# Kernel tuning notes

Measured on AMD Instinct MI355X. Metric: run time of the kernel, lower is better.

## Reference

```python
import jax, jax.numpy as jnp
import numpy as np

B, C_IN, T = 4, 256, 8192
LAYERS, STACKS = 24, 4
RES, GATE, SKIP, K = 128, 256, 128, 3
LPS = LAYERS // STACKS  # layers per stack -> dilation = 2**(i % LPS)
SQRT_HALF = 0.7071067811865476


def setup_inputs() -> dict:
    key = jax.random.key(0)
    ks = jax.random.split(key, 14)
    s = 0.08  # small init so the 24-layer stack stays well-scaled
    inp = {
        "x": jax.random.normal(ks[0], (B, C_IN, T), jnp.float32),
        "first_w": jax.random.normal(ks[1], (RES, C_IN), jnp.float32) * s,
        "first_b": jnp.zeros((RES,), jnp.float32),
        "conv_w": jax.random.normal(ks[2], (LAYERS, GATE, RES, K), jnp.float32) * s,
        "conv_b": jnp.zeros((LAYERS, GATE), jnp.float32),
        "out_w": jax.random.normal(ks[3], (LAYERS, RES, GATE // 2), jnp.float32) * s,
        "out_b": jnp.zeros((LAYERS, RES), jnp.float32),
        "skip_w": jax.random.normal(ks[4], (LAYERS, SKIP, GATE // 2), jnp.float32) * s,
        "skip_b": jnp.zeros((LAYERS, SKIP), jnp.float32),
        "last1_w": jax.random.normal(ks[5], (SKIP, SKIP), jnp.float32) * s,
        "last1_b": jnp.zeros((SKIP,), jnp.float32),
        "last2_w": jax.random.normal(ks[6], (C_IN, SKIP), jnp.float32) * s,
        "last2_b": jnp.zeros((C_IN,), jnp.float32),
    }
    return inp


def _conv1x1(w, b, h):
    # h: [B, C, T], w: [O, C]
    return jnp.einsum('oc,bct->bot', w, h) + b[None, :, None]


def _causal_dilated_conv(h, w, b, dilation):
    # left pad == torch symmetric pad (k-1)*d followed by crop to first T (causal)
    pad = (K - 1) * dilation
    hp = jnp.pad(h, ((0, 0), (0, 0), (pad, 0)))
    y = jax.lax.conv_general_dilated(
        hp, w, window_strides=(1,), padding='VALID',
        rhs_dilation=(dilation,), dimension_numbers=('NCH', 'OIH', 'NCH'))
    return y + b[None, :, None]


def reference(x, first_w, first_b, conv_w, conv_b, out_w, out_b,
              skip_w, skip_b, last1_w, last1_b, last2_w, last2_b):
    h = _conv1x1(first_w, first_b, x)  # [B, RES, T]
    skips = jnp.zeros((x.shape[0], SKIP, x.shape[-1]), h.dtype)
    for i in range(LAYERS):
        d = 2 ** (i % LPS)
        y = _causal_dilated_conv(h, conv_w[i], conv_b[i], d)  # [B, GATE, T]
        a, g = jnp.split(y, 2, axis=1)
        z = jnp.tanh(a) * jax.nn.sigmoid(g)  # gated tanh*sigmoid
        skips = skips + _conv1x1(skip_w[i], skip_b[i], z)
        h = (_conv1x1(out_w[i], out_b[i], z) + h) * SQRT_HALF  # residual
    skips = skips * (1.0 / LAYERS) ** 0.5
    out = jax.nn.relu(skips)
    out = jax.nn.relu(_conv1x1(last1_w, last1_b, out))
    out = _conv1x1(last2_w, last2_b, out)  # logits [B, 256, T]
    return out
```

## Files before the change

### kernel.cpp

```cpp
#include <hip/hip_runtime.h>

#define B 4
#define CIN 256
#define T 8192
#define NL 24
#define TP (64 + T + 8)
#define TT 64
#define SQRT_HALF 0.70710678118654752f
#define SKIP_SCALE 0.20412414523193150f

typedef unsigned short u16;
typedef __attribute__((ext_vector_type(4))) float f32x4;
typedef __attribute__((ext_vector_type(8))) short s16x8;
typedef __attribute__((ext_vector_type(4))) short s16x4;

__device__ inline u16 f2bf(float f) {
  unsigned u = __float_as_uint(f);
  return (u16)((u + 0x7fffu + ((u >> 16) & 1u)) >> 16);
}

__device__ inline void gload_lds16(const void* g, void* l) {
  __builtin_amdgcn_global_load_lds(
      (const __attribute__((address_space(1))) unsigned*)g,
      (__attribute__((address_space(3))) unsigned*)l, 16, 0, 0);
}

__device__ inline float gate_fn(float a, float g) {
  float e2 = __expf(-2.f * fabsf(a));
  float th = (1.f - e2) * __builtin_amdgcn_rcpf(1.f + e2);
  float sg = __builtin_amdgcn_rcpf(1.f + __expf(-g));
  return copysignf(th, a) * sg;
}

__global__ void cvt_convw(const float* __restrict__ src, u16* __restrict__ dst) {
  int i = blockIdx.x * 256 + threadIdx.x;
  if (i >= NL * 3 * 256 * 128) return;
  int c = i & 127, o = (i >> 7) & 255, kk = (i >> 15) % 3, l = (i >> 15) / 3;
  dst[i] = f2bf(src[(((size_t)l * 256 + o) * 128 + c) * 3 + kk]);
}
__global__ void cvt_sow(const float* __restrict__ skw, const float* __restrict__ otw,
                        u16* __restrict__ dst) {
  int i = blockIdx.x * 256 + threadIdx.x;
  if (i >= NL * 256 * 128) return;
  int c = i & 127, r = (i >> 7) & 255, l = i >> 15;
  float v = (r < 128) ? skw[((size_t)l * 128 + r) * 128 + c]
                      : otw[((size_t)l * 128 + (r - 128)) * 128 + c];
  dst[i] = f2bf(v);
}
__global__ void cvt_plain(const float* __restrict__ s, u16* __restrict__ d, int n) {
  int i = blockIdx.x * 256 + threadIdx.x;
  if (i < n) d[i] = f2bf(s[i]);
}
__global__ void padzero(u16* __restrict__ hb) {
  int i = blockIdx.x * 256 + threadIdx.x;
  if (i >= B * 64 * 128) return;
  int c = i & 127, r = (i >> 7) & 63, b = i >> 13;
  hb[((size_t)b * TP + r) * 128 + c] = 0;
}

__global__ __launch_bounds__(256, 2)
void first_kernel(const float* __restrict__ x, const u16* __restrict__ wf,
                  const float* __restrict__ fb, float* __restrict__ hf,
                  u16* __restrict__ hb) {
  __shared__ u16 xT[64 * 256];
  __shared__ u16 hoT[64 * 128];
  const int tid = threadIdx.x, wv = tid >> 6, lane = tid & 63, lo = lane & 15, hi = lane >> 4;
  const int t0 = blockIdx.x * 64, b = blockIdx.y;

  #pragma unroll
  for (int it = 0; it < 16; it++) {
    int idx = tid + it * 256;
    int c = idx >> 4, t4 = (idx & 15) << 2;
    f32x4 v = *(const f32x4*)(x + ((size_t)b * CIN + c) * T + t0 + t4);
    #pragma unroll
    for (int i = 0; i < 4; i++) {
      int t = t4 + i;
      *(u16*)((char*)xT + t * 512 + ((c * 2) ^ ((t & 7) << 4))) = f2bf(v[i]);
    }
  }
  __syncthreads();

  f32x4 acc[2][4];
  #pragma unroll
  for (int m = 0; m < 2; m++)
    #pragma unroll
    for (int n = 0; n < 4; n++) acc[m][n] = (f32x4){0.f, 0.f, 0.f, 0.f};

  #pragma unroll
  for (int s = 0; s < 8; s++) {
    s16x8 af[2], bf[4];
    #pragma unroll
    for (int m = 0; m < 2; m++)
      af[m] = *(const s16x8*)(wf + (size_t)(wv * 32 + m * 16 + lo) * CIN + s * 32 + hi * 8);
    #pragma unroll
    for (int n = 0; n < 4; n++) {
      int t = n * 16 + lo;
      bf[n] = *(const s16x8*)((const char*)xT + t * 512 + ((s * 64 + hi * 16) ^ ((t & 7) << 4)));
    }
    #pragma unroll
    for (int m = 0; m < 2; m++)
      #pragma unroll
      for (int n = 0; n < 4; n++)
        acc[m][n] = __builtin_amdgcn_mfma_f32_16x16x32_bf16(af[m], bf[n], acc[m][n], 0, 0, 0);
  }

  #pragma unroll
  for (int m = 0; m < 2; m++) {
    int c0 = wv * 32 + m * 16 + hi * 4;
    f32x4 bv = *(const f32x4*)(fb + c0);
    #pragma unroll
    for (int n = 0; n < 4; n++) {
      int t = n * 16 + lo;
      f32x4 h = acc[m][n] + bv;
      *(f32x4*)(hf + ((size_t)b * T + t0 + t) * 128 + c0) = h;
      s16x4 pk;
      #pragma unroll
      for (int j = 0; j < 4; j++) pk[j] = (short)f2bf(h[j]);
      *(s16x4*)((char*)hoT + t * 256 + ((c0 * 2) ^ ((t & 7) << 4))) = pk;
    }
  }
  __syncthreads();
  u16* gd = hb + ((size_t)b * TP + 64 + t0) * 128;
  #pragma unroll
  for (int i = 0; i < 4; i++)
    *(s16x8*)((char*)gd + (tid + i * 256) * 16) = *(const s16x8*)((const char*)hoT + (tid + i * 256) * 16);
}

__global__ __launch_bounds__(512, 4)
void layer_kernel(const u16* __restrict__ hbin, u16* __restrict__ hbout,
                  float* __restrict__ hf, float* __restrict__ skip,
                  const u16* __restrict__ wcv, const float* __restrict__ cb,
                  const u16* __restrict__ wso, const float* __restrict__ sb,
                  const float* __restrict__ ob, int d, int first) {
  __shared__ u16 h_s[128 * 128];
  __shared__ u16 zh[64 * 128];
  const int tid = threadIdx.x, wv = tid >> 6, lane = tid & 63, lo = lane & 15, hi = lane >> 4;
  const int t0 = blockIdx.x * TT, b = blockIdx.y;
  const int R = TT + 2 * d;
  const int nch = (R * 256 + 1023) >> 10;

  const char* src = (const char*)(hbin + ((size_t)b * TP + (64 + t0 - 2 * d)) * 128);
  for (int ch = wv; ch < nch; ch += 8)
    gload_lds16(src + ch * 1024 + lane * 16, (char*)h_s + ch * 1024);
  __syncthreads();

  f32x4 acc[2][4];
  #pragma unroll
  for (int m = 0; m < 2; m++)
    #pragma unroll
    for (int n = 0; n < 4; n++) acc[m][n] = (f32x4){0.f, 0.f, 0.f, 0.f};
  const int oa = wv * 16, og = 128 + wv * 16;

  #pragma unroll
  for (int k = 0; k < 3; k++) {
    const int jb = k * d;
    const int st = ((lo + (k + 6) * d) & 7) << 4;
    #pragma unroll
    for (int s = 0; s < 4; s++) {
      s16x8 af0 = *(const s16x8*)(wcv + ((size_t)(k * 256 + oa + lo)) * 128 + s * 32 + hi * 8);
      s16x8 af1 = *(const s16x8*)(wcv + ((size_t)(k * 256 + og + lo)) * 128 + s * 32 + hi * 8);
      const int cbyte = s * 64 + hi * 16;
      s16x8 bf[4];
      #pragma unroll
      for (int n = 0; n < 4; n++) {
        int j = n * 16 + lo + jb;
        bf[n] = *(const s16x8*)((const char*)h_s + j * 256 + (cbyte ^ st));
      }
      #pragma unroll
      for (int n = 0; n < 4; n++) {
        acc[0][n] = __builtin_amdgcn_mfma_f32_16x16x32_bf16(af0, bf[n], acc[0][n], 0, 0, 0);
        acc[1][n] = __builtin_amdgcn_mfma_f32_16x16x32_bf16(af1, bf[n], acc[1][n], 0, 0, 0);
      }
    }
  }

  {
    f32x4 ba = *(const f32x4*)(cb + oa + hi * 4);
    f32x4 bg = *(const f32x4*)(cb + og + hi * 4);
    #pragma unroll
    for (int n = 0; n < 4; n++) {
      int t = n * 16 + lo;
      s16x4 pk;
      #pragma unroll
      for (int j = 0; j < 4; j++)
        pk[j] = (short)f2bf(gate_fn(acc[0][n][j] + ba[j], acc[1][n][j] + bg[j]));
      *(s16x4*)((char*)zh + t * 256 + (((oa + hi * 4) * 2) ^ ((t & 7) << 4))) = pk;
    }
  }
  __syncthreads();

  #pragma unroll
  for (int m = 0; m < 2; m++)
    #pragma unroll
    for (int n = 0; n < 4; n++) acc[m][n] = (f32x4){0.f, 0.f, 0.f, 0.f};
  const int ro = wv * 32;
  #pragma unroll
  for (int s = 0; s < 4; s++) {
    s16x8 af0 = *(const s16x8*)(wso + (size_t)(ro + lo) * 128 + s * 32 + hi * 8);
    s16x8 af1 = *(const s16x8*)(wso + (size_t)(ro + 16 + lo) * 128 + s * 32 + hi * 8);
    const int cbyte = s * 64 + hi * 16;
    s16x8 bf[4];
    #pragma unroll
    for (int n = 0; n < 4; n++) {
      int t = n * 16 + lo;
      bf[n] = *(const s16x8*)((const char*)zh + t * 256 + (cbyte ^ ((t & 7) << 4)));
    }
    #pragma unroll
    for (int n = 0; n < 4; n++) {
      acc[0][n] = __builtin_amdgcn_mfma_f32_16x16x32_bf16(af0, bf[n], acc[0][n], 0, 0, 0);
      acc[1][n] = __builtin_amdgcn_mfma_f32_16x16x32_bf16(af1, bf[n], acc[1][n], 0, 0, 0);
    }
  }
  __syncthreads();

  if (wv < 4) {
    #pragma unroll
    for (int m = 0; m < 2; m++) {
      int c0 = wv * 32 + m * 16 + hi * 4;
      f32x4 sb4 = *(const f32x4*)(sb + c0);
      #pragma unroll
      for (int n = 0; n < 4; n++) {
        size_t off = ((size_t)b * T + t0 + n * 16 + lo) * 128 + c0;
        f32x4 r = acc[m][n] + sb4;
        if (!first) r += *(const f32x4*)(skip + off);
        *(f32x4*)(skip + off) = r;
      }
    }
  } else {
    #pragma unroll
    for (int m = 0; m < 2; m++) {
      int c0 = (wv - 4) * 32 + m * 16 + hi * 4;
      f32x4 ob4 = *(const f32x4*)(ob + c0);
      #pragma unroll
      for (int n = 0; n < 4; n++) {
        int tl = n * 16 + lo;
        size_t off = ((size_t)b * T + t0 + tl) * 128 + c0;
        f32x4 hn = (acc[m][n] + ob4 + *(const f32x4*)(hf + off)) * SQRT_HALF;
        *(f32x4*)(hf + off) = hn;
        s16x4 pk;
        #pragma unroll
        for (int j = 0; j < 4; j++) pk[j] = (short)f2bf(hn[j]);
        *(s16x4*)((char*)zh + tl * 256 + ((c0 * 2) ^ ((tl & 7) << 4))) = pk;
      }
    }
  }
  __syncthreads();
  u16* gd = hbout + ((size_t)b * TP + 64 + t0) * 128;
  #pragma unroll
  for (int i = 0; i < 2; i++)
    *(s16x8*)((char*)gd + (tid + i * 512) * 16) = *(const s16x8*)((const char*)zh + (tid + i * 512) * 16);
}

__global__ __launch_bounds__(256, 2)
void head1_kernel(const float* __restrict__ skip, const u16* __restrict__ w1,
                  const float* __restrict__ b1, u16* __restrict__ s1) {
  __shared__ u16 sT[64 * 128];
  const int tid = threadIdx.x, wv = tid >> 6, lane = tid & 63, lo = lane & 15, hi = lane >> 4;
  const int t0 = blockIdx.x * 64, b = blockIdx.y;

  #pragma unroll
  for (int it = 0; it < 8; it++) {
    int idx = tid + it * 256;
    int t = idx >> 5, c4 = idx & 31;
    f32x4 v = *(const f32x4*)(skip + ((size_t)b * T + t0 + t) * 128 + c4 * 4);
    s16x4 pk;
    #pragma unroll
    for (int i = 0; i < 4; i++) pk[i] = (short)f2bf(fmaxf(v[i] * SKIP_SCALE, 0.f));
    *(s16x4*)((char*)sT + t * 256 + ((c4 * 8) ^ ((t & 7) << 4))) = pk;
  }
  __syncthreads();

  f32x4 acc[2][4];
  #pragma unroll
  for (int m = 0; m < 2; m++)
    #pragma unroll
    for (int n = 0; n < 4; n++) acc[m][n] = (f32x4){0.f, 0.f, 0.f, 0.f};
  #pragma unroll
  for (int s = 0; s < 4; s++) {
    s16x8 af[2], bf[4];
    #pragma unroll
    for (int m = 0; m < 2; m++)
      af[m] = *(const s16x8*)(w1 + (size_t)(wv * 32 + m * 16 + lo) * 128 + s * 32 + hi * 8);
    #pragma unroll
    for (int n = 0; n < 4; n++) {
      int t = n * 16 + lo;
      bf[n] = *(const s16x8*)((const char*)sT + t * 256 + ((s * 64 + hi * 16) ^ ((t & 7) << 4)));
    }
    #pragma unroll
    for (int m = 0; m < 2; m++)
      #pragma unroll
      for (int n = 0; n < 4; n++)
        acc[m][n] = __builtin_amdgcn_mfma_f32_16x16x32_bf16(af[m], bf[n], acc[m][n], 0, 0, 0);
  }
  #pragma unroll
  for (int m = 0; m < 2; m++) {
    int c0 = wv * 32 + m * 16 + hi * 4;
    f32x4 bv = *(const f32x4*)(b1 + c0);
    #pragma unroll
    for (int n = 0; n < 4; n++) {
      int t = n * 16 + lo;
      s16x4 pk;
      #pragma unroll
      for (int j = 0; j < 4; j++) pk[j] = (short)f2bf(fmaxf(acc[m][n][j] + bv[j], 0.f));
      *(s16x4*)((char*)s1 + ((size_t)b * T + t0 + t) * 256 + ((c0 * 2) ^ ((t & 7) << 4))) = pk;
    }
  }
}

__global__ __launch_bounds__(256, 2)
void head2_kernel(const u16* __restrict__ s1, const u16* __restrict__ w2,
                  const float* __restrict__ b2, float* __restrict__ out) {
  __shared__ u16 s1T[64 * 128];
  const int tid = threadIdx.x, wv = tid >> 6, lane = tid & 63, lo = lane & 15, hi = lane >> 4;
  const int t0 = blockIdx.x * 64, b = blockIdx.y;

  const char* src = (const char*)(s1 + ((size_t)b * T + t0) * 128);
  #pragma unroll
  for (int i = 0; i < 4; i++)
    gload_lds16(src + (wv + i * 4) * 1024 + lane * 16, (char*)s1T + (wv + i * 4) * 1024);
  __syncthreads();

  f32x4 acc[4][4];
  #pragma unroll
  for (int m = 0; m < 4; m++)
    #pragma unroll
    for (int n = 0; n < 4; n++) acc[m][n] = (f32x4){0.f, 0.f, 0.f, 0.f};
  #pragma unroll
  for (int s = 0; s < 4; s++) {
    s16x8 af[4], bf[4];
    #pragma unroll
    for (int m = 0; m < 4; m++)
      af[m] = *(const s16x8*)(w2 + (size_t)(wv * 64 + m * 16 + lo) * 128 + s * 32 + hi * 8);
    #pragma unroll
    for (int n = 0; n < 4; n++) {
      int t = n * 16 + lo;
      bf[n] = *(const s16x8*)((const char*)s1T + t * 256 + ((s * 64 + hi * 16) ^ ((t & 7) << 4)));
    }
    #pragma unroll
    for (int m = 0; m < 4; m++)
      #pragma unroll
      for (int n = 0; n < 4; n++)
        acc[m][n] = __builtin_amdgcn_mfma_f32_16x16x32_bf16(af[m], bf[n], acc[m][n], 0, 0, 0);
  }
  #pragma unroll
  for (int m = 0; m < 4; m++) {
    int c0 = wv * 64 + m * 16 + hi * 4;
    f32x4 bv = *(const f32x4*)(b2 + c0);
    #pragma unroll
    for (int n = 0; n < 4; n++) {
      int t = t0 + n * 16 + lo;
      f32x4 r = acc[m][n] + bv;
      #pragma unroll
      for (int j = 0; j < 4; j++) out[((size_t)b * CIN + c0 + j) * T + t] = r[j];
    }
  }
}

extern "C" void kernel_launch(void* const* d_in, const int* in_sizes, int n_in,
                              void* d_out, int out_size, void* d_ws, size_t ws_size,
                              hipStream_t stream) {
  const float* x       = (const float*)d_in[0];
  const float* first_w = (const float*)d_in[1];
  const float* first_b = (const float*)d_in[2];
  const float* conv_w  = (const float*)d_in[3];
  const float* conv_b  = (const float*)d_in[4];
  const float* out_w   = (const float*)d_in[5];
  const float* out_b   = (const float*)d_in[6];
  const float* skip_w  = (const float*)d_in[7];
  const float* skip_b  = (const float*)d_in[8];
  const float* last1_w = (const float*)d_in[9];
  const float* last1_b = (const float*)d_in[10];
  const float* last2_w = (const float*)d_in[11];
  const float* last2_b = (const float*)d_in[12];
  float* out = (float*)d_out;

  u16* wsp  = (u16*)d_ws;
  u16* wcv  = wsp;
  u16* wsoB = wcv + (size_t)NL * 3 * 256 * 128;
  u16* wfB  = wsoB + (size_t)NL * 256 * 128;
  u16* w1B  = wfB + 128 * 256;
  u16* w2B  = w1B + 128 * 128;
  u16* hb0  = w2B + 256 * 128;
  u16* hb1  = hb0 + (size_t)B * TP * 128;
  u16* s1   = hb0;

  float* hf   = (float*)d_out;
  float* skip = hf + (size_t)B * T * 128;

  cvt_convw<<<NL * 3 * 256 * 128 / 256, 256, 0, stream>>>(conv_w, wcv);
  cvt_sow<<<NL * 256 * 128 / 256, 256, 0, stream>>>(skip_w, out_w, wsoB);
  cvt_plain<<<128, 256, 0, stream>>>(first_w, wfB, 128 * 256);
  cvt_plain<<<64, 256, 0, stream>>>(last1_w, w1B, 128 * 128);
  cvt_plain<<<128, 256, 0, stream>>>(last2_w, w2B, 256 * 128);
  padzero<<<128, 256, 0, stream>>>(hb0);
  padzero<<<128, 256, 0, stream>>>(hb1);

  dim3 g64(T / 64, B), gL(T / TT, B);
  first_kernel<<<g64, 256, 0, stream>>>(x, wfB, first_b, hf, hb0);
  for (int i = 0; i < NL; i++) {
    int d = 1 << (i % 6);
    layer_kernel<<<gL, 512, 0, stream>>>(
        (i & 1) ? hb1 : hb0, (i & 1) ? hb0 : hb1, hf, skip,
        wcv + (size_t)i * 3 * 256 * 128, conv_b + (size_t)i * 256,
        wsoB + (size_t)i * 256 * 128, skip_b + (size_t)i * 128,
        out_b + (size_t)i * 128, d, i == 0 ? 1 : 0);
  }
  head1_kernel<<<g64, 256, 0, stream>>>(skip, w1B, last1_b, s1);
  head2_kernel<<<g64, 256, 0, stream>>>(s1, w2B, last2_b, out);
}
```

Measured before the change: 759.2 us.

## Fuse layer pairs into one kernel with recomputed halo and fused head

Replaces the per-layer kernel with a pair kernel that runs two consecutive WaveNet layers per launch. It recomputes the first layer over a 64-step left halo so the second layer's dilated taps are available in LDS, halving launches and global h round-trips. It also drops the bf16 h copy in favor of converting fp32 h on load, merges weight-conversion launches, folds skip biases into one summed vector, and fuses the two head convolutions into one kernel. The cost is the extra halo compute in the first layer of each pair and higher LDS use per block.

```diff
diff --git a/kernel.cpp b/kernel.cpp
--- a/kernel.cpp
+++ b/kernel.cpp
@@ -4,9 +4,7 @@
 #define CIN 256
 #define T 8192
 #define NL 24
-#define TP (64 + T + 8)
-#define TT 64
-#define SQRT_HALF 0.70710678118654752f
+#define SH 0.70710678118654752f
 #define SKIP_SCALE 0.20412414523193150f
 
 typedef unsigned short u16;
@@ -18,13 +16,6 @@
   unsigned u = __float_as_uint(f);
   return (u16)((u + 0x7fffu + ((u >> 16) & 1u)) >> 16);
 }
-
-__device__ inline void gload_lds16(const void* g, void* l) {
-  __builtin_amdgcn_global_load_lds(
-      (const __attribute__((address_space(1))) unsigned*)g,
-      (__attribute__((address_space(3))) unsigned*)l, 16, 0, 0);
-}
-
 __device__ inline float gate_fn(float a, float g) {
   float e2 = __expf(-2.f * fabsf(a));
   float th = (1.f - e2) * __builtin_amdgcn_rcpf(1.f + e2);
@@ -32,38 +23,43 @@
   return copysignf(th, a) * sg;
 }
 
-__global__ void cvt_convw(const float* __restrict__ src, u16* __restrict__ dst) {
+__global__ void cvt_all(const float* __restrict__ conv_w, const float* __restrict__ skip_w,
+                        const float* __restrict__ out_w, const float* __restrict__ first_w,
+                        const float* __restrict__ last1_w, const float* __restrict__ last2_w,
+                        u16* __restrict__ wcv, u16* __restrict__ wso, u16* __restrict__ wf,
+                        u16* __restrict__ w1, u16* __restrict__ w2) {
   int i = blockIdx.x * 256 + threadIdx.x;
-  if (i >= NL * 3 * 256 * 128) return;
-  int c = i & 127, o = (i >> 7) & 255, kk = (i >> 15) % 3, l = (i >> 15) / 3;
-  dst[i] = f2bf(src[(((size_t)l * 256 + o) * 128 + c) * 3 + kk]);
-}
-__global__ void cvt_sow(const float* __restrict__ skw, const float* __restrict__ otw,
-                        u16* __restrict__ dst) {
-  int i = blockIdx.x * 256 + threadIdx.x;
-  if (i >= NL * 256 * 128) return;
-  int c = i & 127, r = (i >> 7) & 255, l = i >> 15;
-  float v = (r < 128) ? skw[((size_t)l * 128 + r) * 128 + c]
-                      : otw[((size_t)l * 128 + (r - 128)) * 128 + c];
-  dst[i] = f2bf(v);
-}
-__global__ void cvt_plain(const float* __restrict__ s, u16* __restrict__ d, int n) {
-  int i = blockIdx.x * 256 + threadIdx.x;
-  if (i < n) d[i] = f2bf(s[i]);
-}
-__global__ void padzero(u16* __restrict__ hb) {
-  int i = blockIdx.x * 256 + threadIdx.x;
-  if (i >= B * 64 * 128) return;
-  int c = i & 127, r = (i >> 7) & 63, b = i >> 13;
-  hb[((size_t)b * TP + r) * 128 + c] = 0;
+  if (i < 2359296) {
+    int c = i & 127, o = (i >> 7) & 255, kk = (i >> 15) % 3, l = (i >> 15) / 3;
+    wcv[i] = f2bf(conv_w[(((size_t)l * 256 + o) * 128 + c) * 3 + kk]);
+    return;
+  }
+  i -= 2359296;
+  if (i < 786432) {
+    int c = i & 127, r = (i >> 7) & 255, l = i >> 15;
+    float v = (r < 128) ? skip_w[((size_t)l * 128 + r) * 128 + c]
+                        : out_w[((size_t)l * 128 + (r - 128)) * 128 + c];
+    wso[i] = f2bf(v);
+    return;
+  }
+  i -= 786432;
+  if (i < 32768) { wf[i] = f2bf(first_w[i]); return; }
+  i -= 32768;
+  if (i < 16384) { w1[i] = f2bf(last1_w[i]); return; }
+  i -= 16384;
+  if (i < 32768) { w2[i] = f2bf(last2_w[i]); return; }
+}
+__global__ void sumsb_kernel(const float* __restrict__ sb, float* __restrict__ dst) {
+  int c = threadIdx.x;
+  float s = 0.f;
+  for (int l = 0; l < NL; l++) s += sb[l * 128 + c];
+  dst[c] = s;
 }
 
 __global__ __launch_bounds__(256, 2)
 void first_kernel(const float* __restrict__ x, const u16* __restrict__ wf,
-                  const float* __restrict__ fb, float* __restrict__ hf,
-                  u16* __restrict__ hb) {
+                  const float* __restrict__ fb, float* __restrict__ hf) {
   __shared__ u16 xT[64 * 256];
-  __shared__ u16 hoT[64 * 128];
   const int tid = threadIdx.x, wv = tid >> 6, lane = tid & 63, lo = lane & 15, hi = lane >> 4;
   const int t0 = blockIdx.x * 64, b = blockIdx.y;
 
@@ -85,7 +81,6 @@
   for (int m = 0; m < 2; m++)
     #pragma unroll
     for (int n = 0; n < 4; n++) acc[m][n] = (f32x4){0.f, 0.f, 0.f, 0.f};
-
   #pragma unroll
   for (int s = 0; s < 8; s++) {
     s16x8 af[2], bf[4];
@@ -103,7 +98,6 @@
       for (int n = 0; n < 4; n++)
         acc[m][n] = __builtin_amdgcn_mfma_f32_16x16x32_bf16(af[m], bf[n], acc[m][n], 0, 0, 0);
   }
-
   #pragma unroll
   for (int m = 0; m < 2; m++) {
     int c0 = wv * 32 + m * 16 + hi * 4;
@@ -111,247 +105,349 @@
     #pragma unroll
     for (int n = 0; n < 4; n++) {
       int t = n * 16 + lo;
-      f32x4 h = acc[m][n] + bv;
-      *(f32x4*)(hf + ((size_t)b * T + t0 + t) * 128 + c0) = h;
+      *(f32x4*)(hf + ((size_t)b * T + t0 + t) * 128 + c0) = acc[m][n] + bv;
+    }
+  }
+}
+
+__global__ __launch_bounds__(512, 4)
+void pair_kernel(const float* __restrict__ hf_in, float* __restrict__ hf_out,
+                 float* __restrict__ skip,
+                 const u16* __restrict__ wc1, const float* __restrict__ cb1,
+                 const u16* __restrict__ ws1, const float* __restrict__ ob1,
+                 const u16* __restrict__ wc2, const float* __restrict__ cb2,
+                 const u16* __restrict__ ws2, const float* __restrict__ ob2,
+                 int d1, int d2, int first) {
+  extern __shared__ u16 lds[];
+  u16* h_s = lds;
+  u16* zh  = lds + 160 * 128;
+  const int tid = threadIdx.x, wv = tid >> 6, lane = tid & 63, lo = lane & 15, hi = lane >> 4;
+  const int tj = blockIdx.x, b = blockIdx.y, t0 = tj * 64;
+  const int R0 = 128 + 2 * d1;
+
+  for (int p = tid; p < R0 * 32; p += 512) {
+    int j0 = p >> 5, cq = p & 31;
+    int t = t0 - 64 - 2 * d1 + j0;
+    f32x4 v = (f32x4){0.f, 0.f, 0.f, 0.f};
+    if (t >= 0) v = *(const f32x4*)(hf_in + ((size_t)b * T + t) * 128 + cq * 4);
+    s16x4 pk;
+    #pragma unroll
+    for (int j = 0; j < 4; j++) pk[j] = (short)f2bf(v[j]);
+    *(s16x4*)((char*)h_s + j0 * 256 + ((cq * 8) ^ (((j0 + 64 - 2 * d1) & 7) << 4))) = pk;
+  }
+  __syncthreads();
+
+  f32x4 A[2][8];
+  const int oa = wv * 16, og = 128 + wv * 16;
+
+  #pragma unroll
+  for (int m = 0; m < 2; m++)
+    #pragma unroll
+    for (int n = 0; n < 8; n++) A[m][n] = (f32x4){0.f, 0.f, 0.f, 0.f};
+  #pragma unroll
+  for (int k = 0; k < 3; k++) {
+    const int st = ((lo + (k + 6) * d1) & 7) << 4;
+    const int jb = k * d1;
+    #pragma unroll
+    for (int s = 0; s < 4; s++) {
+      s16x8 af0 = *(const s16x8*)(wc1 + ((size_t)(k * 256 + oa + lo)) * 128 + s * 32 + hi * 8);
+      s16x8 af1 = *(const s16x8*)(wc1 + ((size_t)(k * 256 + og + lo)) * 128 + s * 32 + hi * 8);
+      const int cb_ = s * 64 + hi * 16;
+      #pragma unroll
+      for (int h2 = 0; h2 < 2; h2++) {
+        s16x8 bf[4];
+        #pragma unroll
+        for (int nn = 0; nn < 4; nn++) {
+          int j0 = (h2 * 4 + nn) * 16 + lo + jb;
+          bf[nn] = *(const s16x8*)((const char*)h_s + j0 * 256 + (cb_ ^ st));
+        }
+        #pragma unroll
+        for (int nn = 0; nn < 4; nn++) {
+          A[0][h2 * 4 + nn] = __builtin_amdgcn_mfma_f32_16x16x32_bf16(af0, bf[nn], A[0][h2 * 4 + nn], 0, 0, 0);
+          A[1][h2 * 4 + nn] = __builtin_amdgcn_mfma_f32_16x16x32_bf16(af1, bf[nn], A[1][h2 * 4 + nn], 0, 0, 0);
+        }
+      }
+    }
+  }
+  {
+    f32x4 ba = *(const f32x4*)(cb1 + oa + hi * 4);
+    f32x4 bg = *(const f32x4*)(cb1 + og + hi * 4);
+    #pragma unroll
+    for (int n = 0; n < 8; n++) {
+      int u = n * 16 + lo;
       s16x4 pk;
       #pragma unroll
-      for (int j = 0; j < 4; j++) pk[j] = (short)f2bf(h[j]);
-      *(s16x4*)((char*)hoT + t * 256 + ((c0 * 2) ^ ((t & 7) << 4))) = pk;
-    }
-  }
-  __syncthreads();
-  u16* gd = hb + ((size_t)b * TP + 64 + t0) * 128;
-  #pragma unroll
-  for (int i = 0; i < 4; i++)
-    *(s16x8*)((char*)gd + (tid + i * 256) * 16) = *(const s16x8*)((const char*)hoT + (tid + i * 256) * 16);
-}
-
-__global__ __launch_bounds__(512, 4)
-void layer_kernel(const u16* __restrict__ hbin, u16* __restrict__ hbout,
-                  float* __restrict__ hf, float* __restrict__ skip,
-                  const u16* __restrict__ wcv, const float* __restrict__ cb,
-                  const u16* __restrict__ wso, const float* __restrict__ sb,
-                  const float* __restrict__ ob, int d, int first) {
-  __shared__ u16 h_s[128 * 128];
-  __shared__ u16 zh[64 * 128];
-  const int tid = threadIdx.x, wv = tid >> 6, lane = tid & 63, lo = lane & 15, hi = lane >> 4;
-  const int t0 = blockIdx.x * TT, b = blockIdx.y;
-  const int R = TT + 2 * d;
-  const int nch = (R * 256 + 1023) >> 10;
-
-  const char* src = (const char*)(hbin + ((size_t)b * TP + (64 + t0 - 2 * d)) * 128);
-  for (int ch = wv; ch < nch; ch += 8)
-    gload_lds16(src + ch * 1024 + lane * 16, (char*)h_s + ch * 1024);
-  __syncthreads();
-
-  f32x4 acc[2][4];
+      for (int j = 0; j < 4; j++)
+        pk[j] = (short)f2bf(gate_fn(A[0][n][j] + ba[j], A[1][n][j] + bg[j]));
+      *(s16x4*)((char*)zh + u * 256 + (((oa + hi * 4) * 2) ^ ((lo & 7) << 4))) = pk;
+    }
+  }
+  __syncthreads();
+
+  const int ro = wv * 32;
+  if (wv < 4) {
+    #pragma unroll
+    for (int m = 0; m < 2; m++)
+      #pragma unroll
+      for (int nn = 0; nn < 4; nn++) A[m][nn + 4] = (f32x4){0.f, 0.f, 0.f, 0.f};
+    #pragma unroll
+    for (int s = 0; s < 4; s++) {
+      s16x8 af0 = *(const s16x8*)(ws1 + (size_t)(ro + lo) * 128 + s * 32 + hi * 8);
+      s16x8 af1 = *(const s16x8*)(ws1 + (size_t)(ro + 16 + lo) * 128 + s * 32 + hi * 8);
+      const int cb_ = s * 64 + hi * 16;
+      s16x8 bf[4];
+      #pragma unroll
+      for (int nn = 0; nn < 4; nn++) {
+        int u = (nn + 4) * 16 + lo;
+        bf[nn] = *(const s16x8*)((const char*)zh + u * 256 + (cb_ ^ ((lo & 7) << 4)));
+      }
+      #pragma unroll
+      for (int nn = 0; nn < 4; nn++) {
+        A[0][nn + 4] = __builtin_amdgcn_mfma_f32_16x16x32_bf16(af0, bf[nn], A[0][nn + 4], 0, 0, 0);
+        A[1][nn + 4] = __builtin_amdgcn_mfma_f32_16x16x32_bf16(af1, bf[nn], A[1][nn + 4], 0, 0, 0);
+      }
+    }
+  } else {
+    #pragma unroll
+    for (int m = 0; m < 2; m++)
+      #pragma unroll
+      for (int n = 0; n < 8; n++) A[m][n] = (f32x4){0.f, 0.f, 0.f, 0.f};
+    #pragma unroll
+    for (int s = 0; s < 4; s++) {
+      s16x8 af0 = *(const s16x8*)(ws1 + (size_t)(ro + lo) * 128 + s * 32 + hi * 8);
+      s16x8 af1 = *(const s16x8*)(ws1 + (size_t)(ro + 16 + lo) * 128 + s * 32 + hi * 8);
+      const int cb_ = s * 64 + hi * 16;
+      #pragma unroll
+      for (int h2 = 0; h2 < 2; h2++) {
+        s16x8 bf[4];
+        #pragma unroll
+        for (int nn = 0; nn < 4; nn++) {
+          int u = (h2 * 4 + nn) * 16 + lo;
+          bf[nn] = *(const s16x8*)((const char*)zh + u * 256 + (cb_ ^ ((lo & 7) << 4)));
+        }
+        #pragma unroll
+        for (int nn = 0; nn < 4; nn++) {
+          A[0][h2 * 4 + nn] = __builtin_amdgcn_mfma_f32_16x16x32_bf16(af0, bf[nn], A[0][h2 * 4 + nn], 0, 0, 0);
+          A[1][h2 * 4 + nn] = __builtin_amdgcn_mfma_f32_16x16x32_bf16(af1, bf[nn], A[1][h2 * 4 + nn], 0, 0, 0);
+        }
+      }
+    }
+    #pragma unroll
+    for (int m = 0; m < 2; m++) {
+      int c0 = (wv - 4) * 32 + m * 16 + hi * 4;
+      f32x4 ob4 = *(const f32x4*)(ob1 + c0);
+      #pragma unroll
+      for (int n = 0; n < 8; n++) {
+        int u = n * 16 + lo;
+        int t_out = t0 - 64 + u;
+        f32x4 h0 = (f32x4){0.f, 0.f, 0.f, 0.f};
+        if (t_out >= 0) h0 = *(const f32x4*)(hf_in + ((size_t)b * T + t_out) * 128 + c0);
+        f32x4 h1 = (A[m][n] + ob4 + h0) * SH;
+        if (t_out < 0) h1 = (f32x4){0.f, 0.f, 0.f, 0.f};
+        A[m][n] = h1;
+        s16x4 pk;
+        #pragma unroll
+        for (int j = 0; j < 4; j++) pk[j] = (short)f2bf(h1[j]);
+        *(s16x4*)((char*)h_s + u * 256 + ((c0 * 2) ^ ((lo & 7) << 4))) = pk;
+      }
+    }
+  }
+  __syncthreads();
+
   #pragma unroll
   for (int m = 0; m < 2; m++)
     #pragma unroll
-    for (int n = 0; n < 4; n++) acc[m][n] = (f32x4){0.f, 0.f, 0.f, 0.f};
-  const int oa = wv * 16, og = 128 + wv * 16;
-
+    for (int n = 0; n < 4; n++) A[m][n] = (f32x4){0.f, 0.f, 0.f, 0.f};
   #pragma unroll
   for (int k = 0; k < 3; k++) {
-    const int jb = k * d;
-    const int st = ((lo + (k + 6) * d) & 7) << 4;
-    #pragma unroll
-    for (int s = 0; s < 4; s++) {
-      s16x8 af0 = *(const s16x8*)(wcv + ((size_t)(k * 256 + oa + lo)) * 128 + s * 32 + hi * 8);
-      s16x8 af1 = *(const s16x8*)(wcv + ((size_t)(k * 256 + og + lo)) * 128 + s * 32 + hi * 8);
-      const int cbyte = s * 64 + hi * 16;
+    const int st = ((lo + (k + 6) * d2) & 7) << 4;
+    const int jb2 = 64 - 2 * d2 + k * d2;
+    #pragma unroll
+    for (int s = 0; s < 4; s++) {
+      s16x8 af0 = *(const s16x8*)(wc2 + ((size_t)(k * 256 + oa + lo)) * 128 + s * 32 + hi * 8);
+      s16x8 af1 = *(const s16x8*)(wc2 + ((size_t)(k * 256 + og + lo)) * 128 + s * 32 + hi * 8);
+      const int cb_ = s * 64 + hi * 16;
       s16x8 bf[4];
       #pragma unroll
+      for (int nn = 0; nn < 4; nn++) {
+        int j1 = nn * 16 + lo + jb2;
+        bf[nn] = *(const s16x8*)((const char*)h_s + j1 * 256 + (cb_ ^ st));
+      }
+      #pragma unroll
+      for (int nn = 0; nn < 4; nn++) {
+        A[0][nn] = __builtin_amdgcn_mfma_f32_16x16x32_bf16(af0, bf[nn], A[0][nn], 0, 0, 0);
+        A[1][nn] = __builtin_amdgcn_mfma_f32_16x16x32_bf16(af1, bf[nn], A[1][nn], 0, 0, 0);
+      }
+    }
+  }
+  {
+    f32x4 ba = *(const f32x4*)(cb2 + oa + hi * 4);
+    f32x4 bg = *(const f32x4*)(cb2 + og + hi * 4);
+    #pragma unroll
+    for (int n = 0; n < 4; n++) {
+      int u = n * 16 + lo;
+      s16x4 pk;
+      #pragma unroll
+      for (int j = 0; j < 4; j++)
+        pk[j] = (short)f2bf(gate_fn(A[0][n][j] + ba[j], A[1][n][j] + bg[j]));
+      *(s16x4*)((char*)zh + u * 256 + (((oa + hi * 4) * 2) ^ ((lo & 7) << 4))) = pk;
+    }
+  }
+  __syncthreads();
+
+  if (wv < 4) {
+    #pragma unroll
+    for (int s = 0; s < 4; s++) {
+      s16x8 af0 = *(const s16x8*)(ws2 + (size_t)(ro + lo) * 128 + s * 32 + hi * 8);
+      s16x8 af1 = *(const s16x8*)(ws2 + (size_t)(ro + 16 + lo) * 128 + s * 32 + hi * 8);
+      const int cb_ = s * 64 + hi * 16;
+      s16x8 bf[4];
+      #pragma unroll
+      for (int nn = 0; nn < 4; nn++) {
+        int u = nn * 16 + lo;
+        bf[nn] = *(const s16x8*)((const char*)zh + u * 256 + (cb_ ^ ((lo & 7) << 4)));
+      }
+      #pragma unroll
+      for (int nn = 0; nn < 4; nn++) {
+        A[0][nn + 4] = __builtin_amdgcn_mfma_f32_16x16x32_bf16(af0, bf[nn], A[0][nn + 4], 0, 0, 0);
+        A[1][nn + 4] = __builtin_amdgcn_mfma_f32_16x16x32_bf16(af1, bf[nn], A[1][nn + 4], 0, 0, 0);
+      }
+    }
+    #pragma unroll
+    for (int m = 0; m < 2; m++) {
+      int c0 = ro + m * 16 + hi * 4;
+      #pragma unroll
       for (int n = 0; n < 4; n++) {
-        int j = n * 16 + lo + jb;
-        bf[n] = *(const s16x8*)((const char*)h_s + j * 256 + (cbyte ^ st));
-      }
-      #pragma unroll
-      for (int n = 0; n < 4; n++) {
-        acc[0][n] = __builtin_amdgcn_mfma_f32_16x16x32_bf16(af0, bf[n], acc[0][n], 0, 0, 0);
-        acc[1][n] = __builtin_amdgcn_mfma_f32_16x16x32_bf16(af1, bf[n], acc[1][n], 0, 0, 0);
-      }
-    }
-  }
-
-  {
-    f32x4 ba = *(const f32x4*)(cb + oa + hi * 4);
-    f32x4 bg = *(const f32x4*)(cb + og + hi * 4);
-    #pragma unroll
-    for (int n = 0; n < 4; n++) {
-      int t = n * 16 + lo;
-      s16x4 pk;
-      #pragma unroll
-      for (int j = 0; j < 4; j++)
-        pk[j] = (short)f2bf(gate_fn(acc[0][n][j] + ba[j], acc[1][n][j] + bg[j]));
-      *(s16x4*)((char*)zh + t * 256 + (((oa + hi * 4) * 2) ^ ((t & 7) << 4))) = pk;
-    }
-  }
-  __syncthreads();
-
-  #pragma unroll
-  for (int m = 0; m < 2; m++)
-    #pragma unroll
-    for (int n = 0; n < 4; n++) acc[m][n] = (f32x4){0.f, 0.f, 0.f, 0.f};
-  const int ro = wv * 32;
-  #pragma unroll
-  for (int s = 0; s < 4; s++) {
-    s16x8 af0 = *(const s16x8*)(wso + (size_t)(ro + lo) * 128 + s * 32 + hi * 8);
-    s16x8 af1 = *(const s16x8*)(wso + (size_t)(ro + 16 + lo) * 128 + s * 32 + hi * 8);
-    const int cbyte = s * 64 + hi * 16;
-    s16x8 bf[4];
-    #pragma unroll
-    for (int n = 0; n < 4; n++) {
-      int t = n * 16 + lo;
-      bf[n] = *(const s16x8*)((const char*)zh + t * 256 + (cbyte ^ ((t & 7) << 4)));
-    }
-    #pragma unroll
-    for (int n = 0; n < 4; n++) {
-      acc[0][n] = __builtin_amdgcn_mfma_f32_16x16x32_bf16(af0, bf[n], acc[0][n], 0, 0, 0);
-      acc[1][n] = __builtin_amdgcn_mfma_f32_16x16x32_bf16(af1, bf[n], acc[1][n], 0, 0, 0);
-    }
-  }
-  __syncthreads();
-
-  if (wv < 4) {
-    #pragma unroll
-    for (int m = 0; m < 2; m++) {
-      int c0 = wv * 32 + m * 16 + hi * 4;
-      f32x4 sb4 = *(const f32x4*)(sb + c0);
-      #pragma unroll
-      for (int n = 0; n < 4; n++) {
-        size_t off = ((size_t)b * T + t0 + n * 16 + lo) * 128 + c0;
-        f32x4 r = acc[m][n] + sb4;
+        int t = t0 + n * 16 + lo;
+        size_t off = ((size_t)b * T + t) * 128 + c0;
+        f32x4 r = A[m][n + 4];
         if (!first) r += *(const f32x4*)(skip + off);
         *(f32x4*)(skip + off) = r;
       }
     }
   } else {
     #pragma unroll
+    for (int m = 0; m < 2; m++)
+      #pragma unroll
+      for (int n = 0; n < 4; n++) A[m][n] = (f32x4){0.f, 0.f, 0.f, 0.f};
+    #pragma unroll
+    for (int s = 0; s < 4; s++) {
+      s16x8 af0 = *(const s16x8*)(ws2 + (size_t)(ro + lo) * 128 + s * 32 + hi * 8);
+      s16x8 af1 = *(const s16x8*)(ws2 + (size_t)(ro + 16 + lo) * 128 + s * 32 + hi * 8);
+      const int cb_ = s * 64 + hi * 16;
+      s16x8 bf[4];
+      #pragma unroll
+      for (int nn = 0; nn < 4; nn++) {
+        int u = nn * 16 + lo;
+        bf[nn] = *(const s16x8*)((const char*)zh + u * 256 + (cb_ ^ ((lo & 7) << 4)));
+      }
+      #pragma unroll
+      for (int nn = 0; nn < 4; nn++) {
+        A[0][nn] = __builtin_amdgcn_mfma_f32_16x16x32_bf16(af0, bf[nn], A[0][nn], 0, 0, 0);
+        A[1][nn] = __builtin_amdgcn_mfma_f32_16x16x32_bf16(af1, bf[nn], A[1][nn], 0, 0, 0);
+      }
+    }
+    #pragma unroll
     for (int m = 0; m < 2; m++) {
       int c0 = (wv - 4) * 32 + m * 16 + hi * 4;
-      f32x4 ob4 = *(const f32x4*)(ob + c0);
+      f32x4 ob4 = *(const f32x4*)(ob2 + c0);
       #pragma unroll
       for (int n = 0; n < 4; n++) {
-        int tl = n * 16 + lo;
-        size_t off = ((size_t)b * T + t0 + tl) * 128 + c0;
-        f32x4 hn = (acc[m][n] + ob4 + *(const f32x4*)(hf + off)) * SQRT_HALF;
-        *(f32x4*)(hf + off) = hn;
-        s16x4 pk;
-        #pragma unroll
-        for (int j = 0; j < 4; j++) pk[j] = (short)f2bf(hn[j]);
-        *(s16x4*)((char*)zh + tl * 256 + ((c0 * 2) ^ ((tl & 7) << 4))) = pk;
-      }
-    }
-  }
-  __syncthreads();
-  u16* gd = hbout + ((size_t)b * TP + 64 + t0) * 128;
-  #pragma unroll
-  for (int i = 0; i < 2; i++)
-    *(s16x8*)((char*)gd + (tid + i * 512) * 16) = *(const s16x8*)((const char*)zh + (tid + i * 512) * 16);
+        int t = t0 + n * 16 + lo;
+        f32x4 h2v = (A[m][n] + ob4 + A[m][n + 4]) * SH;
+        *(f32x4*)(hf_out + ((size_t)b * T + t) * 128 + c0) = h2v;
+      }
+    }
+  }
 }
 
 __global__ __launch_bounds__(256, 2)
-void head1_kernel(const float* __restrict__ skip, const u16* __restrict__ w1,
-                  const float* __restrict__ b1, u16* __restrict__ s1) {
+void head_kernel(const float* __restrict__ skip, const float* __restrict__ sumsb,
+                 const u16* __restrict__ w1, const float* __restrict__ b1v,
+                 const u16* __restrict__ w2, const float* __restrict__ b2v,
+                 float* __restrict__ out) {
   __shared__ u16 sT[64 * 128];
-  const int tid = threadIdx.x, wv = tid >> 6, lane = tid & 63, lo = lane & 15, hi = lane >> 4;
-  const int t0 = blockIdx.x * 64, b = blockIdx.y;
-
-  #pragma unroll
-  for (int it = 0; it < 8; it++) {
-    int idx = tid + it * 256;
-    int t = idx >> 5, c4 = idx & 31;
-    f32x4 v = *(const f32x4*)(skip + ((size_t)b * T + t0 + t) * 128 + c4 * 4);
-    s16x4 pk;
-    #pragma unroll
-    for (int i = 0; i < 4; i++) pk[i] = (short)f2bf(fmaxf(v[i] * SKIP_SCALE, 0.f));
-    *(s16x4*)((char*)sT + t * 256 + ((c4 * 8) ^ ((t & 7) << 4))) = pk;
-  }
-  __syncthreads();
-
-  f32x4 acc[2][4];
-  #pragma unroll
-  for (int m = 0; m < 2; m++)
-    #pragma unroll
-    for (int n = 0; n < 4; n++) acc[m][n] = (f32x4){0.f, 0.f, 0.f, 0.f};
-  #pragma unroll
-  for (int s = 0; s < 4; s++) {
-    s16x8 af[2], bf[4];
-    #pragma unroll
-    for (int m = 0; m < 2; m++)
-      af[m] = *(const s16x8*)(w1 + (size_t)(wv * 32 + m * 16 + lo) * 128 + s * 32 + hi * 8);
-    #pragma unroll
-    for (int n = 0; n < 4; n++) {
-      int t = n * 16 + lo;
-      bf[n] = *(const s16x8*)((const char*)sT + t * 256 + ((s * 64 + hi * 16) ^ ((t & 7) << 4)));
-    }
-    #pragma unroll
-    for (int m = 0; m < 2; m++)
-      #pragma unroll
-      for (int n = 0; n < 4; n++)
-        acc[m][n] = __builtin_amdgcn_mfma_f32_16x16x32_bf16(af[m], bf[n], acc[m][n], 0, 0, 0);
-  }
-  #pragma unroll
-  for (int m = 0; m < 2; m++) {
-    int c0 = wv * 32 + m * 16 + hi * 4;
-    f32x4 bv = *(const f32x4*)(b1 + c0);
-    #pragma unroll
-    for (int n = 0; n < 4; n++) {
-      int t = n * 16 + lo;
-      s16x4 pk;
-      #pragma unroll
-      for (int j = 0; j < 4; j++) pk[j] = (short)f2bf(fmaxf(acc[m][n][j] + bv[j], 0.f));
-      *(s16x4*)((char*)s1 + ((size_t)b * T + t0 + t) * 256 + ((c0 * 2) ^ ((t & 7) << 4))) = pk;
-    }
-  }
-}
-
-__global__ __launch_bounds__(256, 2)
-void head2_kernel(const u16* __restrict__ s1, const u16* __restrict__ w2,
-                  const float* __restrict__ b2, float* __restrict__ out) {
   __shared__ u16 s1T[64 * 128];
   const int tid = threadIdx.x, wv = tid >> 6, lane = tid & 63, lo = lane & 15, hi = lane >> 4;
   const int t0 = blockIdx.x * 64, b = blockIdx.y;
 
-  const char* src = (const char*)(s1 + ((size_t)b * T + t0) * 128);
-  #pragma unroll
-  for (int i = 0; i < 4; i++)
-    gload_lds16(src + (wv + i * 4) * 1024 + lane * 16, (char*)s1T + (wv + i * 4) * 1024);
-  __syncthreads();
-
-  f32x4 acc[4][4];
-  #pragma unroll
-  for (int m = 0; m < 4; m++)
-    #pragma unroll
-    for (int n = 0; n < 4; n++) acc[m][n] = (f32x4){0.f, 0.f, 0.f, 0.f};
-  #pragma unroll
-  for (int s = 0; s < 4; s++) {
-    s16x8 af[4], bf[4];
+  #pragma unroll
+  for (int it = 0; it < 8; it++) {
+    int p = tid + it * 256;
+    int t = p >> 5, cq = p & 31;
+    f32x4 v = *(const f32x4*)(skip + ((size_t)b * T + t0 + t) * 128 + cq * 4);
+    f32x4 sb4 = *(const f32x4*)(sumsb + cq * 4);
+    s16x4 pk;
+    #pragma unroll
+    for (int j = 0; j < 4; j++) pk[j] = (short)f2bf(fmaxf((v[j] + sb4[j]) * SKIP_SCALE, 0.f));
+    *(s16x4*)((char*)sT + t * 256 + ((cq * 8) ^ ((t & 7) << 4))) = pk;
+  }
+  __syncthreads();
+  {
+    f32x4 acc[2][4];
+    #pragma unroll
+    for (int m = 0; m < 2; m++)
+      #pragma unroll
+      for (int n = 0; n < 4; n++) acc[m][n] = (f32x4){0.f, 0.f, 0.f, 0.f};
+    #pragma unroll
+    for (int s = 0; s < 4; s++) {
+      s16x8 af0 = *(const s16x8*)(w1 + (size_t)(wv * 32 + lo) * 128 + s * 32 + hi * 8);
+      s16x8 af1 = *(const s16x8*)(w1 + (size_t)(wv * 32 + 16 + lo) * 128 + s * 32 + hi * 8);
+      #pragma unroll
+      for (int n = 0; n < 4; n++) {
+        int t = n * 16 + lo;
+        s16x8 bf = *(const s16x8*)((const char*)sT + t * 256 + ((s * 64 + hi * 16) ^ ((t & 7) << 4)));
+        acc[0][n] = __builtin_amdgcn_mfma_f32_16x16x32_bf16(af0, bf, acc[0][n], 0, 0, 0);
+        acc[1][n] = __builtin_amdgcn_mfma_f32_16x16x32_bf16(af1, bf, acc[1][n], 0, 0, 0);
+      }
+    }
+    #pragma unroll
+    for (int m = 0; m < 2; m++) {
+      int c0 = wv * 32 + m * 16 + hi * 4;
+      f32x4 bv = *(const f32x4*)(b1v + c0);
+      #pragma unroll
+      for (int n = 0; n < 4; n++) {
+        int t = n * 16 + lo;
+        s16x4 pk;
+        #pragma unroll
+        for (int j = 0; j < 4; j++) pk[j] = (short)f2bf(fmaxf(acc[m][n][j] + bv[j], 0.f));
+        *(s16x4*)((char*)s1T + t * 256 + ((c0 * 2) ^ ((t & 7) << 4))) = pk;
+      }
+    }
+  }
+  __syncthreads();
+  {
+    f32x4 acc[4][4];
     #pragma unroll
     for (int m = 0; m < 4; m++)
-      af[m] = *(const s16x8*)(w2 + (size_t)(wv * 64 + m * 16 + lo) * 128 + s * 32 + hi * 8);
-    #pragma unroll
-    for (int n = 0; n < 4; n++) {
-      int t = n * 16 + lo;
-      bf[n] = *(const s16x8*)((const char*)s1T + t * 256 + ((s * 64 + hi * 16) ^ ((t & 7) << 4)));
-    }
-    #pragma unroll
-    for (int m = 0; m < 4; m++)
-      #pragma unroll
-      for (int n = 0; n < 4; n++)
-        acc[m][n] = __builtin_amdgcn_mfma_f32_16x16x32_bf16(af[m], bf[n], acc[m][n], 0, 0, 0);
-  }
-  #pragma unroll
-  for (int m = 0; m < 4; m++) {
-    int c0 = wv * 64 + m * 16 + hi * 4;
-    f32x4 bv = *(const f32x4*)(b2 + c0);
-    #pragma unroll
-    for (int n = 0; n < 4; n++) {
-      int t = t0 + n * 16 + lo;
-      f32x4 r = acc[m][n] + bv;
-      #pragma unroll
-      for (int j = 0; j < 4; j++) out[((size_t)b * CIN + c0 + j) * T + t] = r[j];
+      #pragma unroll
+      for (int n = 0; n < 4; n++) acc[m][n] = (f32x4){0.f, 0.f, 0.f, 0.f};
+    #pragma unroll
+    for (int s = 0; s < 4; s++) {
+      s16x8 af[4];
+      #pragma unroll
+      for (int m = 0; m < 4; m++)
+        af[m] = *(const s16x8*)(w2 + (size_t)(wv * 64 + m * 16 + lo) * 128 + s * 32 + hi * 8);
+      #pragma unroll
+      for (int n = 0; n < 4; n++) {
+        int t = n * 16 + lo;
+        s16x8 bf = *(const s16x8*)((const char*)s1T + t * 256 + ((s * 64 + hi * 16) ^ ((t & 7) << 4)));
+        #pragma unroll
+        for (int m = 0; m < 4; m++)
+          acc[m][n] = __builtin_amdgcn_mfma_f32_16x16x32_bf16(af[m], bf, acc[m][n], 0, 0, 0);
+      }
+    }
+    #pragma unroll
+    for (int m = 0; m < 4; m++) {
+      int c0 = wv * 64 + m * 16 + hi * 4;
+      f32x4 bv = *(const f32x4*)(b2v + c0);
+      #pragma unroll
+      for (int n = 0; n < 4; n++) {
+        int t = t0 + n * 16 + lo;
+        f32x4 r = acc[m][n] + bv;
+        #pragma unroll
+        for (int j = 0; j < 4; j++) out[((size_t)b * CIN + c0 + j) * T + t] = r[j];
+      }
     }
   }
 }
@@ -374,37 +470,35 @@
   const float* last2_b = (const float*)d_in[12];
   float* out = (float*)d_out;
 
-  u16* wsp  = (u16*)d_ws;
-  u16* wcv  = wsp;
-  u16* wsoB = wcv + (size_t)NL * 3 * 256 * 128;
-  u16* wfB  = wsoB + (size_t)NL * 256 * 128;
-  u16* w1B  = wfB + 128 * 256;
-  u16* w2B  = w1B + 128 * 128;
-  u16* hb0  = w2B + 256 * 128;
-  u16* hb1  = hb0 + (size_t)B * TP * 128;
-  u16* s1   = hb0;
-
-  float* hf   = (float*)d_out;
-  float* skip = hf + (size_t)B * T * 128;
-
-  cvt_convw<<<NL * 3 * 256 * 128 / 256, 256, 0, stream>>>(conv_w, wcv);
-  cvt_sow<<<NL * 256 * 128 / 256, 256, 0, stream>>>(skip_w, out_w, wsoB);
-  cvt_plain<<<128, 256, 0, stream>>>(first_w, wfB, 128 * 256);
-  cvt_plain<<<64, 256, 0, stream>>>(last1_w, w1B, 128 * 128);
-  cvt_plain<<<128, 256, 0, stream>>>(last2_w, w2B, 256 * 128);
-  padzero<<<128, 256, 0, stream>>>(hb0);
-  padzero<<<128, 256, 0, stream>>>(hb1);
-
-  dim3 g64(T / 64, B), gL(T / TT, B);
-  first_kernel<<<g64, 256, 0, stream>>>(x, wfB, first_b, hf, hb0);
-  for (int i = 0; i < NL; i++) {
-    int d = 1 << (i % 6);
-    layer_kernel<<<gL, 512, 0, stream>>>(
-        (i & 1) ? hb1 : hb0, (i & 1) ? hb0 : hb1, hf, skip,
-        wcv + (size_t)i * 3 * 256 * 128, conv_b + (size_t)i * 256,
-        wsoB + (size_t)i * 256 * 128, skip_b + (size_t)i * 128,
-        out_b + (size_t)i * 128, d, i == 0 ? 1 : 0);
-  }
-  head1_kernel<<<g64, 256, 0, stream>>>(skip, w1B, last1_b, s1);
-  head2_kernel<<<g64, 256, 0, stream>>>(s1, w2B, last2_b, out);
-}
+  u16* wcv = (u16*)d_ws;
+  u16* wso = wcv + (size_t)NL * 3 * 256 * 128;
+  u16* wf  = wso + (size_t)NL * 256 * 128;
+  u16* w1  = wf + 128 * 256;
+  u16* w2  = w1 + 128 * 128;
+  float* sumsb = (float*)(w2 + 256 * 128);
+  float* skipF = sumsb + 128;
+  float* hfA = (float*)d_out;
+  float* hfB = hfA + (size_t)B * T * 128;
+
+  cvt_all<<<12608, 256, 0, stream>>>(conv_w, skip_w, out_w, first_w, last1_w, last2_w,
+                                     wcv, wso, wf, w1, w2);
+  sumsb_kernel<<<1, 128, 0, stream>>>(skip_b, sumsb);
+
+  dim3 grid(T / 64, B);
+  first_kernel<<<grid, 256, 0, stream>>>(x, wf, first_b, hfA);
+
+  for (int p = 0; p < NL / 2; p++) {
+    int l1 = 2 * p, l2 = 2 * p + 1;
+    int d1 = 1 << (l1 % 6), d2 = 1 << (l2 % 6);
+    const float* hin = (p & 1) ? hfB : hfA;
+    float* hout = (p & 1) ? hfA : hfB;
+    pair_kernel<<<grid, 512, 73728, stream>>>(
+        hin, hout, skipF,
+        wcv + (size_t)l1 * 3 * 256 * 128, conv_b + (size_t)l1 * 256,
+        wso + (size_t)l1 * 256 * 128, out_b + (size_t)l1 * 128,
+        wcv + (size_t)l2 * 3 * 256 * 128, conv_b + (size_t)l2 * 256,
+        wso + (size_t)l2 * 256 * 128, out_b + (size_t)l2 * 128,
+        d1, d2, p == 0 ? 1 : 0);
+  }
+  head_kernel<<<grid, 256, 0, stream>>>(skipF, sumsb, w1, last1_b, w2, last2_b, out);
+}
```

After: 696.8 us. 1.09x faster.
